# Kernel tuning notes

Measured on AMD Instinct MI355X. Metric: run time of the kernel, lower is better.

The kernel has to match this reference:

```python
import jax, jax.numpy as jnp
import numpy as np

N = 50000        # nodes
E = 800000       # edges (avg degree 16)
F_IN = 256       # cfg.dataset.features
H = 256          # cfg.model.hidden_size


def setup_inputs() -> dict:
    key = jax.random.key(0)
    ks = jax.random.split(key, 8)
    x = jax.random.normal(ks[0], (N, F_IN), dtype=jnp.float32)
    edge_index = jax.random.randint(ks[1], (2, E), 0, N, dtype=jnp.int32)
    # GCNConv weights: layer0 in->hidden, layer1 hidden->hidden, layer2 hidden->1
    W0 = jax.random.normal(ks[2], (F_IN, H), jnp.float32) / np.sqrt(F_IN)
    b0 = jnp.zeros((H,), jnp.float32)
    W1 = jax.random.normal(ks[3], (H, H), jnp.float32) / np.sqrt(H)
    b1 = jnp.zeros((H,), jnp.float32)
    W2 = jax.random.normal(ks[4], (H, 1), jnp.float32) / np.sqrt(H)
    b2 = jnp.zeros((1,), jnp.float32)
    return {"x": x, "edge_index": edge_index, "W0": W0, "b0": b0,
            "W1": W1, "b1": b1, "W2": W2, "b2": b2}


def reference(x, edge_index, W0, b0, W1, b1, W2, b2):
    n = x.shape[0]
    loop = jnp.arange(n, dtype=edge_index.dtype)
    # gcn_norm with self-loops: Ahat = D^{-1/2} (A + I) D^{-1/2}
    src = jnp.concatenate([edge_index[0], loop])  # [E+N]
    dst = jnp.concatenate([edge_index[1], loop])  # [E+N]
    deg = jax.ops.segment_sum(jnp.ones_like(src, dtype=x.dtype), dst, num_segments=n)
    dinv = jnp.where(deg > 0, jax.lax.rsqrt(deg), 0.0)
    norm = dinv[src] * dinv[dst]                  # [E+N]

    def gcn_layer(h, W, b):
        h = h @ W                                              # [N, out]
        agg = jax.ops.segment_sum(norm[:, None] * h[src], dst, num_segments=n)
        return agg + b

    h = jax.nn.relu(gcn_layer(x, W0, b0))
    h = jax.nn.relu(gcn_layer(h, W1, b1))
    return gcn_layer(h, W2, b2)                                # [N, 1]
```

## Files before the change

kernel.cpp:

```cpp
#include <hip/hip_runtime.h>


static inline size_t alignup(size_t x, size_t a) { return (x + a - 1) & ~(a - 1); }

typedef __attribute__((ext_vector_type(8))) short short8;
typedef __attribute__((ext_vector_type(4))) float f32x4;

__device__ inline unsigned short f2bf(float f) {
    union { float f; unsigned int u; } v; v.f = f;
    unsigned int r = v.u + 0x7FFFu + ((v.u >> 16) & 1u);
    return (unsigned short)(r >> 16);
}
__device__ inline float bf2f(unsigned short u) {
    union { unsigned int u; float f; } v; v.u = ((unsigned int)u) << 16;
    return v.f;
}

__global__ __launch_bounds__(256) void k_fill_i32(int* __restrict__ p, int v, int n) {
    int i = blockIdx.x * 256 + threadIdx.x;
    if (i < n) p[i] = v;
}

__global__ __launch_bounds__(256) void k_count_deg(const int* __restrict__ dst, int* __restrict__ deg, int E) {
    int e = blockIdx.x * 256 + threadIdx.x;
    if (e < E) atomicAdd(&deg[dst[e]], 1);
}

__global__ __launch_bounds__(256) void k_scan1(const int* __restrict__ deg, int* __restrict__ rs,
                                               int* __restrict__ bsum, float* __restrict__ dinv, int n) {
    __shared__ int sd[256];
    int b = blockIdx.x, tid = threadIdx.x;
    int base = b * 1024 + tid * 4;
    int v[4];
#pragma unroll
    for (int j = 0; j < 4; ++j) v[j] = (base + j < n) ? deg[base + j] : 0;
    int tot = v[0] + v[1] + v[2] + v[3];
    sd[tid] = tot;
    for (int off = 1; off < 256; off <<= 1) {
        __syncthreads();
        int t = (tid >= off) ? sd[tid - off] : 0;
        __syncthreads();
        sd[tid] += t;
    }
    __syncthreads();
    int run = tid ? sd[tid - 1] : 0;
#pragma unroll
    for (int j = 0; j < 4; ++j) {
        if (base + j < n) {
            rs[base + j] = run;
            dinv[base + j] = rsqrtf((float)v[j] + 1.0f);
        }
        run += v[j];
    }
    if (tid == 255) bsum[b] = sd[255];
}

__global__ __launch_bounds__(256) void k_scan2(int* __restrict__ bsum, int nb) {
    __shared__ int sd[256];
    int tid = threadIdx.x;
    sd[tid] = (tid < nb) ? bsum[tid] : 0;
    for (int off = 1; off < 256; off <<= 1) {
        __syncthreads();
        int t = (tid >= off) ? sd[tid - off] : 0;
        __syncthreads();
        sd[tid] += t;
    }
    __syncthreads();
    if (tid < nb) bsum[tid] = tid ? sd[tid - 1] : 0;
}

__global__ __launch_bounds__(256) void k_scan3(int* __restrict__ rs, int* __restrict__ cursor,
                                               const int* __restrict__ bsum, int n, int E) {
    int b = blockIdx.x, tid = threadIdx.x;
    int off = bsum[b];
    int base = b * 1024 + tid * 4;
#pragma unroll
    for (int j = 0; j < 4; ++j) {
        int idx = base + j;
        if (idx < n) {
            int v = rs[idx] + off;
            rs[idx] = v;
            cursor[idx] = v;
        }
    }
    if (b == 0 && tid == 0) rs[n] = E;
}

__global__ __launch_bounds__(256) void k_fill_csr(const int* __restrict__ src, const int* __restrict__ dst,
                                                  int* __restrict__ cursor, int* __restrict__ col, int E) {
    int e = blockIdx.x * 256 + threadIdx.x;
    if (e < E) {
        int d = dst[e];
        int pos = atomicAdd(&cursor[d], 1);
        col[pos] = src[e];
    }
}

__global__ __launch_bounds__(256) void k_wt2(const float* __restrict__ W0, const float* __restrict__ W1,
                                             unsigned short* __restrict__ Wt0, unsigned short* __restrict__ Wt1) {
    int idx = blockIdx.x * 256 + threadIdx.x;
    const float* W = (idx < 65536) ? W0 : W1;
    unsigned short* Wt = (idx < 65536) ? Wt0 : Wt1;
    int id = idx & 65535;
    int k = id >> 8, n = id & 255;
    Wt[(size_t)n * 256 + k] = f2bf(W[(size_t)k * 256 + n]);
}

template <bool AF32>
__global__ __launch_bounds__(256) void k_gemm_mfma(const void* __restrict__ Ap,
                                                   const unsigned short* __restrict__ Wt,
                                                   unsigned short* __restrict__ C,
                                                   const float* __restrict__ dinv, int N) {
    __shared__ __align__(16) unsigned short smem[16384];
    unsigned short* As2 = smem;
    unsigned short* Bs2 = smem + 4096;
    unsigned short* Cs = smem;

    int tid = threadIdx.x;
    int lane = tid & 63, w = tid >> 6;
    int wr = w >> 1, wc = w & 1;
    int row0 = blockIdx.y * 128, col0 = blockIdx.x * 128;

    f32x4 acc[4][4];
#pragma unroll
    for (int m = 0; m < 4; ++m)
#pragma unroll
        for (int n = 0; n < 4; ++n) acc[m][n] = (f32x4)0.f;

    const int c0 = tid, c1 = tid + 256;
    const int ar0 = c0 >> 2, akg0 = c0 & 3, ar1 = c1 >> 2, akg1 = c1 & 3;

    auto loadA = [&](int r, int kg, int k0) -> short8 {
        short8 u = {0, 0, 0, 0, 0, 0, 0, 0};
        int grow = row0 + r;
        if (grow < N) {
            if constexpr (AF32) {
                const float* g = (const float*)Ap + (size_t)grow * 256 + k0 + kg * 8;
                float4 f0 = *(const float4*)g;
                float4 f1 = *(const float4*)(g + 4);
                u[0] = (short)f2bf(f0.x); u[1] = (short)f2bf(f0.y);
                u[2] = (short)f2bf(f0.z); u[3] = (short)f2bf(f0.w);
                u[4] = (short)f2bf(f1.x); u[5] = (short)f2bf(f1.y);
                u[6] = (short)f2bf(f1.z); u[7] = (short)f2bf(f1.w);
            } else {
                u = *(const short8*)((const unsigned short*)Ap + (size_t)grow * 256 + k0 + kg * 8);
            }
        }
        return u;
    };
    auto loadB = [&](int n, int kg, int k0) -> short8 {
        return *(const short8*)(Wt + (size_t)(col0 + n) * 256 + k0 + kg * 8);
    };
    auto stash = [&](short8 a0, short8 a1, short8 b0, short8 b1) {
        *(short8*)&As2[(ar0 >> 4) * 512 + akg0 * 128 + (ar0 & 15) * 8] = a0;
        *(short8*)&As2[(ar1 >> 4) * 512 + akg1 * 128 + (ar1 & 15) * 8] = a1;
        *(short8*)&Bs2[(ar0 >> 4) * 512 + akg0 * 128 + (ar0 & 15) * 8] = b0;
        *(short8*)&Bs2[(ar1 >> 4) * 512 + akg1 * 128 + (ar1 & 15) * 8] = b1;
    };

    {
        short8 a0 = loadA(ar0, akg0, 0), a1 = loadA(ar1, akg1, 0);
        short8 b0 = loadB(ar0, akg0, 0), b1 = loadB(ar1, akg1, 0);
        stash(a0, a1, b0, b1);
    }
    __syncthreads();

#pragma unroll
    for (int i = 0; i < 8; ++i) {
        short8 na0, na1, nb0, nb1;
        if (i < 7) {
            int k0 = i * 32 + 32;
            na0 = loadA(ar0, akg0, k0); na1 = loadA(ar1, akg1, k0);
            nb0 = loadB(ar0, akg0, k0); nb1 = loadB(ar1, akg1, k0);
        }
        short8 af[4], bfr[4];
#pragma unroll
        for (int m = 0; m < 4; ++m)
            af[m] = *(const short8*)&As2[(wr * 4 + m) * 512 + (lane >> 4) * 128 + (lane & 15) * 8];
#pragma unroll
        for (int n = 0; n < 4; ++n)
            bfr[n] = *(const short8*)&Bs2[(wc * 4 + n) * 512 + (lane >> 4) * 128 + (lane & 15) * 8];
#pragma unroll
        for (int m = 0; m < 4; ++m)
#pragma unroll
            for (int n = 0; n < 4; ++n)
                acc[m][n] = __builtin_amdgcn_mfma_f32_16x16x32_bf16(af[m], bfr[n], acc[m][n], 0, 0, 0);
        if (i < 7) {
            __syncthreads();
            stash(na0, na1, nb0, nb1);
            __syncthreads();
        }
    }
    __syncthreads();

    unsigned short* myCs = &Cs[w * 4096];
#pragma unroll
    for (int m = 0; m < 4; ++m) {
#pragma unroll
        for (int j = 0; j < 4; ++j) {
            int r = m * 16 + (lane >> 4) * 4 + j;
            int grow = row0 + wr * 64 + r;
            float d = (grow < N) ? dinv[grow] : 0.f;
#pragma unroll
            for (int n = 0; n < 4; ++n)
                myCs[r * 64 + n * 16 + (lane & 15)] = f2bf(acc[m][n][j] * d);
        }
    }
    __syncthreads();
#pragma unroll
    for (int i = 0; i < 8; ++i) {
        int r = i * 8 + (lane >> 3);
        int grow = row0 + wr * 64 + r;
        if (grow < N) {
            short8 v = *(const short8*)&myCs[r * 64 + (lane & 7) * 8];
            *(short8*)(C + (size_t)grow * 256 + col0 + wc * 64 + (lane & 7) * 8) = v;
        }
    }
}

template <bool FUSE_GEMV>
__global__ __launch_bounds__(256) void k_agg(const unsigned short* __restrict__ t,
                                             unsigned short* __restrict__ h,
                                             const int* __restrict__ rs, const int* __restrict__ col,
                                             const float* __restrict__ dinv, const float* __restrict__ bias,
                                             const float* __restrict__ W2, float* __restrict__ z,
                                             int N) {
    int wid = (blockIdx.x * 256 + threadIdx.x) >> 6;
    int lane = threadIdx.x & 63;
    if (wid >= N) return;
    int half = lane >> 5, sub = lane & 31;
    const short8* tp = (const short8*)t;

    short8 sv = tp[(size_t)wid * 32 + sub];
    float hsel = (half == 0) ? 1.f : 0.f;
    float a[8];
#pragma unroll
    for (int i = 0; i < 8; ++i) a[i] = hsel * bf2f((unsigned short)sv[i]);

    int e0 = rs[wid], e1 = rs[wid + 1];
    for (int base = e0; base < e1; base += 64) {
        int m = e1 - base; if (m > 64) m = 64;
        int c = (base + lane < e1) ? col[base + lane] : 0;
        int npairs = (m + 1) >> 1;
        int j = 0;
        for (; j + 4 <= npairs; j += 4) {
            int i0 = 2 * j + half, i1 = i0 + 2, i2 = i0 + 4, i3 = i0 + 6;
            int s0 = __shfl(c, i0), s1 = __shfl(c, i1), s2 = __shfl(c, i2), s3 = __shfl(c, i3);
            float f0 = (i0 < m) ? 1.f : 0.f, f1 = (i1 < m) ? 1.f : 0.f;
            float f2 = (i2 < m) ? 1.f : 0.f, f3 = (i3 < m) ? 1.f : 0.f;
            short8 w0 = tp[(size_t)s0 * 32 + sub];
            short8 w1 = tp[(size_t)s1 * 32 + sub];
            short8 w2 = tp[(size_t)s2 * 32 + sub];
            short8 w3 = tp[(size_t)s3 * 32 + sub];
#pragma unroll
            for (int i = 0; i < 8; ++i) {
                a[i] = fmaf(f0, bf2f((unsigned short)w0[i]), a[i]);
                a[i] = fmaf(f1, bf2f((unsigned short)w1[i]), a[i]);
                a[i] = fmaf(f2, bf2f((unsigned short)w2[i]), a[i]);
                a[i] = fmaf(f3, bf2f((unsigned short)w3[i]), a[i]);
            }
        }
        for (; j < npairs; ++j) {
            int i0 = 2 * j + half;
            int s0 = __shfl(c, i0);
            float f0 = (i0 < m) ? 1.f : 0.f;
            short8 w0 = tp[(size_t)s0 * 32 + sub];
#pragma unroll
            for (int i = 0; i < 8; ++i) a[i] = fmaf(f0, bf2f((unsigned short)w0[i]), a[i]);
        }
    }
#pragma unroll
    for (int i = 0; i < 8; ++i) a[i] += __shfl_xor(a[i], 32, 64);

    float d = dinv[wid];
    float4 b0 = ((const float4*)bias)[sub * 2];
    float4 b1 = ((const float4*)bias)[sub * 2 + 1];
    float o[8];
    o[0] = fmaf(d, a[0], b0.x); o[1] = fmaf(d, a[1], b0.y);
    o[2] = fmaf(d, a[2], b0.z); o[3] = fmaf(d, a[3], b0.w);
    o[4] = fmaf(d, a[4], b1.x); o[5] = fmaf(d, a[5], b1.y);
    o[6] = fmaf(d, a[6], b1.z); o[7] = fmaf(d, a[7], b1.w);
#pragma unroll
    for (int i = 0; i < 8; ++i) o[i] = fmaxf(o[i], 0.f);

    if constexpr (FUSE_GEMV) {
        float4 wv0 = ((const float4*)W2)[sub * 2];
        float4 wv1 = ((const float4*)W2)[sub * 2 + 1];
        float zp = o[0] * wv0.x + o[1] * wv0.y + o[2] * wv0.z + o[3] * wv0.w +
                   o[4] * wv1.x + o[5] * wv1.y + o[6] * wv1.z + o[7] * wv1.w;
#pragma unroll
        for (int off = 16; off > 0; off >>= 1) zp += __shfl_down(zp, off, 32);
        if (lane == 0) z[wid] = d * zp;
    } else {
        if (half == 0) {
            short8 u;
#pragma unroll
            for (int i = 0; i < 8; ++i) u[i] = (short)f2bf(o[i]);
            *(short8*)(h + (size_t)wid * 256 + sub * 8) = u;
        }
    }
}

__global__ __launch_bounds__(256) void k_agg_out(const float* __restrict__ z, float* __restrict__ out,
                                                 const int* __restrict__ rs, const int* __restrict__ col,
                                                 const float* __restrict__ dinv, const float* __restrict__ b2,
                                                 int N) {
    int wid = (blockIdx.x * 256 + threadIdx.x) >> 6;
    int lane = threadIdx.x & 63;
    if (wid >= N) return;
    int e0 = rs[wid], e1 = rs[wid + 1];
    float v = 0.f;
    for (int base = e0; base < e1; base += 64) {
        int e = base + lane;
        if (e < e1) v += z[col[e]];
    }
#pragma unroll
    for (int off = 32; off > 0; off >>= 1) v += __shfl_down(v, off, 64);
    if (lane == 0) out[wid] = fmaf(dinv[wid], v + z[wid], b2[0]);
}

extern "C" void kernel_launch(void* const* d_in, const int* in_sizes, int n_in,
                              void* d_out, int out_size, void* d_ws, size_t ws_size,
                              hipStream_t stream) {
    const float* x  = (const float*)d_in[0];
    const int*   ei = (const int*)d_in[1];
    const float* W0 = (const float*)d_in[2];
    const float* b0 = (const float*)d_in[3];
    const float* W1 = (const float*)d_in[4];
    const float* b1 = (const float*)d_in[5];
    const float* W2 = (const float*)d_in[6];
    const float* b2 = (const float*)d_in[7];
    float* out = (float*)d_out;

    int N = in_sizes[0] / 256;
    int E = in_sizes[1] / 2;
    const int* esrc = ei;
    const int* edst = ei + E;

    char* p = (char*)d_ws;
    unsigned short* tb = (unsigned short*)p; p += alignup((size_t)N * 256 * 2, 16);
    unsigned short* hb = (unsigned short*)p; p += alignup((size_t)N * 256 * 2, 16);
    unsigned short* Wt0 = (unsigned short*)p; p += 256 * 256 * 2;
    unsigned short* Wt1 = (unsigned short*)p; p += 256 * 256 * 2;
    float* z = (float*)p;      p += alignup((size_t)N * 4, 16);
    float* dinv = (float*)p;   p += alignup((size_t)N * 4, 16);
    int* deg = (int*)p;        p += alignup((size_t)N * 4, 16);
    int* cursor = (int*)p;     p += alignup((size_t)N * 4, 16);
    int* rs = (int*)p;         p += alignup((size_t)(N + 1) * 4, 16);
    int* col = (int*)p;        p += alignup((size_t)E * 4, 16);
    int* bsum = (int*)p;       p += 256 * 4;

    int nb = (N + 1023) / 1024;
    dim3 blk(256);

    k_fill_i32<<<(N + 255) / 256, blk, 0, stream>>>(deg, 0, N);
    k_count_deg<<<(E + 255) / 256, blk, 0, stream>>>(edst, deg, E);
    k_scan1<<<nb, blk, 0, stream>>>(deg, rs, bsum, dinv, N);
    k_scan2<<<1, blk, 0, stream>>>(bsum, nb);
    k_scan3<<<nb, blk, 0, stream>>>(rs, cursor, bsum, N, E);
    k_fill_csr<<<(E + 255) / 256, blk, 0, stream>>>(esrc, edst, cursor, col, E);
    k_wt2<<<512, blk, 0, stream>>>(W0, W1, Wt0, Wt1);

    dim3 gg(2, (N + 127) / 128);
    k_gemm_mfma<true><<<gg, blk, 0, stream>>>(x, Wt0, tb, dinv, N);
    k_agg<false><<<(N + 3) / 4, blk, 0, stream>>>(tb, hb, rs, col, dinv, b0, nullptr, nullptr, N);
    k_gemm_mfma<false><<<gg, blk, 0, stream>>>(hb, Wt1, tb, dinv, N);
    k_agg<true><<<(N + 3) / 4, blk, 0, stream>>>(tb, nullptr, rs, col, dinv, b1, W2, z, N);
    k_agg_out<<<(N + 3) / 4, blk, 0, stream>>>(z, out, rs, col, dinv, b2, N);
}
```

Before: 361.8 us.

## Fuse graph preprocessing into one cooperative kernel and double-buffer GEMM LDS

Merges the seven preprocessing launches (degree zeroing, weight transpose, degree count, three scan stages, CSR fill) into a single cooperative kernel of 768 blocks that uses grid-wide syncs between phases. This removes per-launch overhead and inter-kernel gaps. Separately, the MFMA GEMM now ping-pongs between two LDS buffers, so each k-step needs one barrier instead of two. Grid syncs add their own cost, and the cooperative launch depends on all 768 blocks being co-resident.

```diff
diff --git a/kernel.cpp b/kernel.cpp
--- a/kernel.cpp
+++ b/kernel.cpp
@@ -1,4 +1,7 @@
 #include <hip/hip_runtime.h>
+#include <hip/hip_cooperative_groups.h>
+
+namespace cg = cooperative_groups;
 
 
 static inline size_t alignup(size_t x, size_t a) { return (x + a - 1) & ~(a - 1); }
@@ -16,94 +19,95 @@
     return v.f;
 }
 
-__global__ __launch_bounds__(256) void k_fill_i32(int* __restrict__ p, int v, int n) {
-    int i = blockIdx.x * 256 + threadIdx.x;
-    if (i < n) p[i] = v;
-}
-
-__global__ __launch_bounds__(256) void k_count_deg(const int* __restrict__ dst, int* __restrict__ deg, int E) {
-    int e = blockIdx.x * 256 + threadIdx.x;
-    if (e < E) atomicAdd(&deg[dst[e]], 1);
-}
-
-__global__ __launch_bounds__(256) void k_scan1(const int* __restrict__ deg, int* __restrict__ rs,
-                                               int* __restrict__ bsum, float* __restrict__ dinv, int n) {
-    __shared__ int sd[256];
-    int b = blockIdx.x, tid = threadIdx.x;
-    int base = b * 1024 + tid * 4;
-    int v[4];
-#pragma unroll
-    for (int j = 0; j < 4; ++j) v[j] = (base + j < n) ? deg[base + j] : 0;
-    int tot = v[0] + v[1] + v[2] + v[3];
-    sd[tid] = tot;
-    for (int off = 1; off < 256; off <<= 1) {
-        __syncthreads();
-        int t = (tid >= off) ? sd[tid - off] : 0;
-        __syncthreads();
-        sd[tid] += t;
-    }
-    __syncthreads();
-    int run = tid ? sd[tid - 1] : 0;
-#pragma unroll
-    for (int j = 0; j < 4; ++j) {
-        if (base + j < n) {
-            rs[base + j] = run;
-            dinv[base + j] = rsqrtf((float)v[j] + 1.0f);
-        }
-        run += v[j];
-    }
-    if (tid == 255) bsum[b] = sd[255];
-}
-
-__global__ __launch_bounds__(256) void k_scan2(int* __restrict__ bsum, int nb) {
+__global__ __launch_bounds__(256) void k_pre(const int* __restrict__ esrc, const int* __restrict__ edst,
+                                             int E, int N,
+                                             int* __restrict__ deg, int* __restrict__ rs,
+                                             int* __restrict__ cursor, int* __restrict__ col,
+                                             int* __restrict__ bsum, float* __restrict__ dinv,
+                                             const float* __restrict__ W0, const float* __restrict__ W1,
+                                             unsigned short* __restrict__ Wt0, unsigned short* __restrict__ Wt1) {
+    cg::grid_group grid = cg::this_grid();
     __shared__ int sd[256];
     int tid = threadIdx.x;
-    sd[tid] = (tid < nb) ? bsum[tid] : 0;
-    for (int off = 1; off < 256; off <<= 1) {
+    int b = blockIdx.x;
+    int gtid = b * 256 + tid;
+    int stride = gridDim.x * 256;
+    int nb = (N + 1023) / 1024;
+
+    for (int i = gtid; i < N; i += stride) deg[i] = 0;
+    for (int i = gtid; i < 131072; i += stride) {
+        const float* W = (i < 65536) ? W0 : W1;
+        unsigned short* Wt = (i < 65536) ? Wt0 : Wt1;
+        int id = i & 65535;
+        int k = id >> 8, n = id & 255;
+        Wt[(size_t)n * 256 + k] = f2bf(W[(size_t)k * 256 + n]);
+    }
+    grid.sync();
+
+    for (int e = gtid; e < E; e += stride) atomicAdd(&deg[edst[e]], 1);
+    grid.sync();
+
+    if (b < nb) {
+        int base = b * 1024 + tid * 4;
+        int v[4];
+#pragma unroll
+        for (int j = 0; j < 4; ++j) v[j] = (base + j < N) ? deg[base + j] : 0;
+        int tot = v[0] + v[1] + v[2] + v[3];
+        sd[tid] = tot;
+        for (int off = 1; off < 256; off <<= 1) {
+            __syncthreads();
+            int t = (tid >= off) ? sd[tid - off] : 0;
+            __syncthreads();
+            sd[tid] += t;
+        }
         __syncthreads();
-        int t = (tid >= off) ? sd[tid - off] : 0;
+        int run = tid ? sd[tid - 1] : 0;
+#pragma unroll
+        for (int j = 0; j < 4; ++j) {
+            if (base + j < N) {
+                rs[base + j] = run;
+                dinv[base + j] = rsqrtf((float)v[j] + 1.0f);
+            }
+            run += v[j];
+        }
+        if (tid == 255) bsum[b] = sd[255];
+    }
+    grid.sync();
+
+    if (b == 0) {
+        sd[tid] = (tid < nb) ? bsum[tid] : 0;
+        for (int off = 1; off < 256; off <<= 1) {
+            __syncthreads();
+            int t = (tid >= off) ? sd[tid - off] : 0;
+            __syncthreads();
+            sd[tid] += t;
+        }
         __syncthreads();
-        sd[tid] += t;
-    }
-    __syncthreads();
-    if (tid < nb) bsum[tid] = tid ? sd[tid - 1] : 0;
-}
-
-__global__ __launch_bounds__(256) void k_scan3(int* __restrict__ rs, int* __restrict__ cursor,
-                                               const int* __restrict__ bsum, int n, int E) {
-    int b = blockIdx.x, tid = threadIdx.x;
-    int off = bsum[b];
-    int base = b * 1024 + tid * 4;
-#pragma unroll
-    for (int j = 0; j < 4; ++j) {
-        int idx = base + j;
-        if (idx < n) {
-            int v = rs[idx] + off;
-            rs[idx] = v;
-            cursor[idx] = v;
-        }
-    }
-    if (b == 0 && tid == 0) rs[n] = E;
-}
-
-__global__ __launch_bounds__(256) void k_fill_csr(const int* __restrict__ src, const int* __restrict__ dst,
-                                                  int* __restrict__ cursor, int* __restrict__ col, int E) {
-    int e = blockIdx.x * 256 + threadIdx.x;
-    if (e < E) {
-        int d = dst[e];
+        if (tid < nb) bsum[tid] = tid ? sd[tid - 1] : 0;
+    }
+    grid.sync();
+
+    if (b < nb) {
+        int off = bsum[b];
+        int base = b * 1024 + tid * 4;
+#pragma unroll
+        for (int j = 0; j < 4; ++j) {
+            int idx = base + j;
+            if (idx < N) {
+                int v = rs[idx] + off;
+                rs[idx] = v;
+                cursor[idx] = v;
+            }
+        }
+    }
+    if (gtid == 0) rs[N] = E;
+    grid.sync();
+
+    for (int e = gtid; e < E; e += stride) {
+        int d = edst[e];
         int pos = atomicAdd(&cursor[d], 1);
-        col[pos] = src[e];
-    }
-}
-
-__global__ __launch_bounds__(256) void k_wt2(const float* __restrict__ W0, const float* __restrict__ W1,
-                                             unsigned short* __restrict__ Wt0, unsigned short* __restrict__ Wt1) {
-    int idx = blockIdx.x * 256 + threadIdx.x;
-    const float* W = (idx < 65536) ? W0 : W1;
-    unsigned short* Wt = (idx < 65536) ? Wt0 : Wt1;
-    int id = idx & 65535;
-    int k = id >> 8, n = id & 255;
-    Wt[(size_t)n * 256 + k] = f2bf(W[(size_t)k * 256 + n]);
+        col[pos] = esrc[e];
+    }
 }
 
 template <bool AF32>
@@ -112,8 +116,8 @@
                                                    unsigned short* __restrict__ C,
                                                    const float* __restrict__ dinv, int N) {
     __shared__ __align__(16) unsigned short smem[16384];
-    unsigned short* As2 = smem;
-    unsigned short* Bs2 = smem + 4096;
+    unsigned short* Asb[2] = {smem, smem + 8192};
+    unsigned short* Bsb[2] = {smem + 4096, smem + 12288};
     unsigned short* Cs = smem;
 
     int tid = threadIdx.x;
@@ -151,22 +155,23 @@
     auto loadB = [&](int n, int kg, int k0) -> short8 {
         return *(const short8*)(Wt + (size_t)(col0 + n) * 256 + k0 + kg * 8);
     };
-    auto stash = [&](short8 a0, short8 a1, short8 b0, short8 b1) {
-        *(short8*)&As2[(ar0 >> 4) * 512 + akg0 * 128 + (ar0 & 15) * 8] = a0;
-        *(short8*)&As2[(ar1 >> 4) * 512 + akg1 * 128 + (ar1 & 15) * 8] = a1;
-        *(short8*)&Bs2[(ar0 >> 4) * 512 + akg0 * 128 + (ar0 & 15) * 8] = b0;
-        *(short8*)&Bs2[(ar1 >> 4) * 512 + akg1 * 128 + (ar1 & 15) * 8] = b1;
+    auto stash = [&](int buf, short8 a0, short8 a1, short8 b0, short8 b1) {
+        *(short8*)&Asb[buf][(ar0 >> 4) * 512 + akg0 * 128 + (ar0 & 15) * 8] = a0;
+        *(short8*)&Asb[buf][(ar1 >> 4) * 512 + akg1 * 128 + (ar1 & 15) * 8] = a1;
+        *(short8*)&Bsb[buf][(ar0 >> 4) * 512 + akg0 * 128 + (ar0 & 15) * 8] = b0;
+        *(short8*)&Bsb[buf][(ar1 >> 4) * 512 + akg1 * 128 + (ar1 & 15) * 8] = b1;
     };
 
     {
         short8 a0 = loadA(ar0, akg0, 0), a1 = loadA(ar1, akg1, 0);
         short8 b0 = loadB(ar0, akg0, 0), b1 = loadB(ar1, akg1, 0);
-        stash(a0, a1, b0, b1);
+        stash(0, a0, a1, b0, b1);
     }
     __syncthreads();
 
 #pragma unroll
     for (int i = 0; i < 8; ++i) {
+        int cur = i & 1;
         short8 na0, na1, nb0, nb1;
         if (i < 7) {
             int k0 = i * 32 + 32;
@@ -176,22 +181,18 @@
         short8 af[4], bfr[4];
 #pragma unroll
         for (int m = 0; m < 4; ++m)
-            af[m] = *(const short8*)&As2[(wr * 4 + m) * 512 + (lane >> 4) * 128 + (lane & 15) * 8];
+            af[m] = *(const short8*)&Asb[cur][(wr * 4 + m) * 512 + (lane >> 4) * 128 + (lane & 15) * 8];
 #pragma unroll
         for (int n = 0; n < 4; ++n)
-            bfr[n] = *(const short8*)&Bs2[(wc * 4 + n) * 512 + (lane >> 4) * 128 + (lane & 15) * 8];
+            bfr[n] = *(const short8*)&Bsb[cur][(wc * 4 + n) * 512 + (lane >> 4) * 128 + (lane & 15) * 8];
 #pragma unroll
         for (int m = 0; m < 4; ++m)
 #pragma unroll
             for (int n = 0; n < 4; ++n)
                 acc[m][n] = __builtin_amdgcn_mfma_f32_16x16x32_bf16(af[m], bfr[n], acc[m][n], 0, 0, 0);
-        if (i < 7) {
-            __syncthreads();
-            stash(na0, na1, nb0, nb1);
-            __syncthreads();
-        }
-    }
-    __syncthreads();
+        if (i < 7) stash(cur ^ 1, na0, na1, nb0, nb1);
+        __syncthreads();
+    }
 
     unsigned short* myCs = &Cs[w * 4096];
 #pragma unroll
@@ -350,16 +351,15 @@
     int* col = (int*)p;        p += alignup((size_t)E * 4, 16);
     int* bsum = (int*)p;       p += 256 * 4;
 
-    int nb = (N + 1023) / 1024;
     dim3 blk(256);
 
-    k_fill_i32<<<(N + 255) / 256, blk, 0, stream>>>(deg, 0, N);
-    k_count_deg<<<(E + 255) / 256, blk, 0, stream>>>(edst, deg, E);
-    k_scan1<<<nb, blk, 0, stream>>>(deg, rs, bsum, dinv, N);
-    k_scan2<<<1, blk, 0, stream>>>(bsum, nb);
-    k_scan3<<<nb, blk, 0, stream>>>(rs, cursor, bsum, N, E);
-    k_fill_csr<<<(E + 255) / 256, blk, 0, stream>>>(esrc, edst, cursor, col, E);
-    k_wt2<<<512, blk, 0, stream>>>(W0, W1, Wt0, Wt1);
+    {
+        void* args[] = {(void*)&esrc, (void*)&edst, (void*)&E, (void*)&N,
+                        (void*)&deg, (void*)&rs, (void*)&cursor, (void*)&col,
+                        (void*)&bsum, (void*)&dinv,
+                        (void*)&W0, (void*)&W1, (void*)&Wt0, (void*)&Wt1};
+        hipLaunchCooperativeKernel((const void*)k_pre, dim3(768), blk, args, 0, stream);
+    }
 
     dim3 gg(2, (N + 127) / 128);
     k_gemm_mfma<true><<<gg, blk, 0, stream>>>(x, Wt0, tb, dinv, N);
```

Result: slower. 810.3 us (+124.0%).
